# Optimization experiments

Hardware: AMD Instinct MI355X
Metric: run time of the kernel (lower is better)

## Reference

```python
import jax, jax.numpy as jnp
import numpy as np

DEPTH = 10
LAMDA = 1e-3
EPS = 1e-7


def setup_inputs() -> dict:
    key = jax.random.key(0)
    k1, k2, k3, k4 = jax.random.split(key, 4)
    B, D, O = 16384, 512, 256
    N = 2 ** DEPTH - 1        # inner nodes
    L = 2 ** DEPTH            # leaves
    data = jax.random.normal(k1, (B, D), jnp.float32)
    # small scale on W keeps sigmoid away from saturation (like nn.Linear init)
    W = jax.random.normal(k2, (N, D + 1), jnp.float32) * 0.02
    beta = jax.random.normal(k3, (N,), jnp.float32)
    param = jax.random.normal(k4, (L, O), jnp.float32)
    return {"data": data, "W": W, "beta": beta, "param": param}


def reference(data, W, beta, param):
    B = data.shape[0]
    L = param.shape[0]
    # _data_augment_: prepend constant 1 as bias feature -> [B, D+1]
    x = jnp.concatenate([jnp.ones((B, 1), data.dtype), data], axis=1)
    # inner_nodes: sigmoid(beta * linear(x)) -> [B, N]
    p = jax.nn.sigmoid(beta * (x @ W.T))
    # per-node (go-left, go-right) probabilities -> [B, N, 2]
    path_prob = jnp.stack([p, 1.0 - p], axis=2)

    mu = jnp.ones((B, 1), data.dtype)          # path prob of root
    penalty = jnp.asarray(0.0, data.dtype)
    begin = 0
    for layer in range(DEPTH):                  # fixed small loop over depth
        n = 2 ** layer
        pp = path_prob[:, begin:begin + n, :].reshape(B, 2 * n)  # [B, 2n]
        mu_rep = jnp.repeat(mu, 2, axis=1)                        # [B, 2n]
        # vectorized form of the per-node penalty loop
        alpha = jnp.sum(pp * mu_rep, axis=0) / (jnp.sum(mu_rep, axis=0) + EPS)
        alpha = jnp.clip(alpha, EPS, 1.0 - EPS)
        coeff = LAMDA * (2.0 ** (-layer))
        penalty = penalty - coeff * 0.5 * jnp.sum(jnp.log(alpha) + jnp.log(1.0 - alpha))
        mu = mu_rep * pp
        begin += n

    # mu: [B, leaf_num]; leaf_nodes: mu @ softmax(param)
    dist = jax.nn.softmax(param, axis=1)       # [L, O]
    output = mu @ dist                          # [B, O]
    # greatest_path_probability: hard argmax leaf (one-hot @ dist == gather)
    ids = jnp.argmax(mu, axis=1)
    prediction = dist[ids]                      # [B, O]
    # LogProb=True
    return (jnp.log(prediction), jnp.log(output), penalty, W)
```

## Files before the change

### kernel.cpp

```cpp
#include <hip/hip_runtime.h>
#include <hip/hip_bf16.h>

#define B_ROWS 16384
#define DDIM   512
#define NNODES 1023
#define NLEAF  1024
#define ODIM   256
#define LAMDA  1e-3
#define EPSV   1e-7f

typedef __bf16 bf16x8v __attribute__((ext_vector_type(8)));
typedef _Float16 f16x8 __attribute__((ext_vector_type(8)));
typedef float  f32x16v __attribute__((ext_vector_type(16)));

__device__ __forceinline__ float bf2f(unsigned short u) {
    return __uint_as_float(((unsigned)u) << 16);
}

__device__ __forceinline__ void gload16h(const _Float16* g, _Float16* l) {
    __builtin_amdgcn_global_load_lds(
        (const __attribute__((address_space(1))) unsigned int*)g,
        (__attribute__((address_space(3))) unsigned int*)l, 16, 0, 0);
}
__device__ __forceinline__ void gload16b(const __hip_bfloat16* g, __hip_bfloat16* l) {
    __builtin_amdgcn_global_load_lds(
        (const __attribute__((address_space(1))) unsigned int*)g,
        (__attribute__((address_space(3))) unsigned int*)l, 16, 0, 0);
}

__global__ __launch_bounds__(256)
void prep_data(const float* __restrict__ data,
               _Float16* __restrict__ Dh, _Float16* __restrict__ Dl)
{
    int idx = blockIdx.x * 256 + threadIdx.x;
    int b  = idx >> 6;
    int k8 = idx & 63;
    const float4 v0 = *reinterpret_cast<const float4*>(&data[(size_t)b * DDIM + k8 * 8]);
    const float4 v1 = *reinterpret_cast<const float4*>(&data[(size_t)b * DDIM + k8 * 8 + 4]);
    float a[8] = {v0.x, v0.y, v0.z, v0.w, v1.x, v1.y, v1.z, v1.w};
    __align__(16) _Float16 h[8], l[8];
#pragma unroll
    for (int j = 0; j < 8; ++j) {
        h[j] = (_Float16)a[j];
        l[j] = (_Float16)((a[j] - (float)h[j]) * 2048.f);
    }
    int by = b >> 7, tl = (b >> 5) & 3, ln = (b & 31) | ((k8 & 1) << 5), ks = k8 >> 1;
    size_t off = ((((size_t)by * 32 + ks) * 4 + tl) * 64 + ln) * 8;
    *reinterpret_cast<ulonglong2*>(&Dh[off]) = *reinterpret_cast<const ulonglong2*>(h);
    *reinterpret_cast<ulonglong2*>(&Dl[off]) = *reinterpret_cast<const ulonglong2*>(l);
}

__global__ __launch_bounds__(256)
void prep_w(const float* __restrict__ W,
            _Float16* __restrict__ Wh, _Float16* __restrict__ Wl)
{
    int idx = blockIdx.x * 256 + threadIdx.x;
    int t  = idx & 255;
    int ks = (idx >> 8) & 31;
    int nb = idx >> 13;
    int tm = t >> 6, ln = t & 63;
    int node = nb * 128 + tm * 32 + (ln & 31);
    int k = ks * 16 + (ln >> 5) * 8;
    __align__(16) _Float16 h[8], l[8];
    if (node < NNODES) {
#pragma unroll
        for (int j = 0; j < 8; ++j) {
            float a = W[(size_t)node * 513 + 1 + k + j];
            h[j] = (_Float16)a;
            l[j] = (_Float16)((a - (float)h[j]) * 2048.f);
        }
    } else {
#pragma unroll
        for (int j = 0; j < 8; ++j) { h[j] = (_Float16)0.f; l[j] = (_Float16)0.f; }
    }
    size_t off = (size_t)idx * 8;
    *reinterpret_cast<ulonglong2*>(&Wh[off]) = *reinterpret_cast<const ulonglong2*>(h);
    *reinterpret_cast<ulonglong2*>(&Wl[off]) = *reinterpret_cast<const ulonglong2*>(l);
}

__global__ __launch_bounds__(256, 2)
void gemm1_mfma(const _Float16* __restrict__ Wh, const _Float16* __restrict__ Wl,
                const _Float16* __restrict__ Dh, const _Float16* __restrict__ Dl,
                const float* __restrict__ W, const float* __restrict__ beta,
                float* __restrict__ PT)
{
    __shared__ _Float16 lds[2][4][4096];
    const int tid = threadIdx.x;
    const int lane = tid & 63;
    const int wv = tid >> 6;
    const int wm = wv & 1, wn = wv >> 1;
    const int id = blockIdx.x;
    const int xcd = id & 7, slot = id >> 3;
    const int bx = slot & 7;
    const int by = xcd * 16 + (slot >> 3);
    const size_t wofs = (size_t)bx * 65536 + tid * 8;
    const size_t dofs = (size_t)by * 65536 + tid * 8;
    const int t16 = tid * 8;

    f32x16v acc_h[2][2] = {};
    f32x16v acc_l[2][2] = {};

#define STAGE1(buf, tt) do { \
        const size_t so = (size_t)(tt) * 4096; \
        gload16h(Wh + wofs + so,        &lds[buf][0][t16]); \
        gload16h(Wh + wofs + so + 2048, &lds[buf][0][2048 + t16]); \
        gload16h(Wl + wofs + so,        &lds[buf][1][t16]); \
        gload16h(Wl + wofs + so + 2048, &lds[buf][1][2048 + t16]); \
        gload16h(Dh + dofs + so,        &lds[buf][2][t16]); \
        gload16h(Dh + dofs + so + 2048, &lds[buf][2][2048 + t16]); \
        gload16h(Dl + dofs + so,        &lds[buf][3][t16]); \
        gload16h(Dl + dofs + so + 2048, &lds[buf][3][2048 + t16]); \
    } while (0)

    STAGE1(0, 0);

    for (int t = 0; t < 16; ++t) {
        const int cur = t & 1;
        if (t + 1 < 16) {
            STAGE1(cur ^ 1, t + 1);
            asm volatile("s_waitcnt vmcnt(8)" ::: "memory");
        } else {
            asm volatile("s_waitcnt vmcnt(0)" ::: "memory");
        }
        __builtin_amdgcn_s_barrier();

        f16x8 ah[2][2], al[2][2], bh[2][2], bl[2][2];
#pragma unroll
        for (int kcl = 0; kcl < 2; ++kcl)
#pragma unroll
            for (int i = 0; i < 2; ++i) {
                int ao = kcl * 2048 + (wm * 2 + i) * 512 + lane * 8;
                int bo = kcl * 2048 + (wn * 2 + i) * 512 + lane * 8;
                ah[kcl][i] = *reinterpret_cast<const f16x8*>(&lds[cur][0][ao]);
                al[kcl][i] = *reinterpret_cast<const f16x8*>(&lds[cur][1][ao]);
                bh[kcl][i] = *reinterpret_cast<const f16x8*>(&lds[cur][2][bo]);
                bl[kcl][i] = *reinterpret_cast<const f16x8*>(&lds[cur][3][bo]);
            }
        __builtin_amdgcn_s_setprio(1);
#pragma unroll
        for (int kcl = 0; kcl < 2; ++kcl)
#pragma unroll
            for (int i = 0; i < 2; ++i)
#pragma unroll
                for (int j = 0; j < 2; ++j) {
                    acc_h[i][j] = __builtin_amdgcn_mfma_f32_32x32x16_f16(ah[kcl][i], bh[kcl][j], acc_h[i][j], 0, 0, 0);
                    acc_l[i][j] = __builtin_amdgcn_mfma_f32_32x32x16_f16(ah[kcl][i], bl[kcl][j], acc_l[i][j], 0, 0, 0);
                    acc_l[i][j] = __builtin_amdgcn_mfma_f32_32x32x16_f16(al[kcl][i], bh[kcl][j], acc_l[i][j], 0, 0, 0);
                }
        __builtin_amdgcn_s_setprio(0);
        asm volatile("s_waitcnt lgkmcnt(0)" ::: "memory");
        __builtin_amdgcn_s_barrier();
    }
#undef STAGE1

#pragma unroll
    for (int i = 0; i < 2; ++i) {
#pragma unroll
        for (int r = 0; r < 16; ++r) {
            int node = bx * 128 + wm * 64 + i * 32 + ((r & 3) + 8 * (r >> 2) + 4 * (lane >> 5));
            if (node < NNODES) {
                float w0 = W[(size_t)node * 513];
                float bt = beta[node];
#pragma unroll
                for (int j = 0; j < 2; ++j) {
                    float z = acc_h[i][j][r] + acc_l[i][j][r] * 4.8828125e-4f;
                    float s = bt * (z + w0);
                    float p = 1.f / (1.f + expf(-s));
                    PT[(size_t)node * B_ROWS + by * 128 + wn * 64 + j * 32 + (lane & 31)] = p;
                }
            }
        }
    }
}

__global__ __launch_bounds__(256, 4)
void tree_pass(const float* __restrict__ PT,
               __hip_bfloat16* __restrict__ MU2,
               float* __restrict__ pval,
               int*   __restrict__ pidx)
{
    const int tid = threadIdx.x;
    const int rb = blockIdx.x & 63;
    const int g  = blockIdx.x >> 6;
    const int b  = rb * 256 + tid;

    const int c4 = 15 + g;
    const int n3 = (c4 - 1) >> 1;
    const int n2 = (n3 - 1) >> 1;
    const int n1 = (n2 - 1) >> 1;
    const float pc4 = PT[(size_t)c4 * B_ROWS + b];
    const float pn3 = PT[(size_t)n3 * B_ROWS + b];
    const float pn2 = PT[(size_t)n2 * B_ROWS + b];
    const float pn1 = PT[(size_t)n1 * B_ROWS + b];
    const float pn0 = PT[b];
    float pre = ((c4 & 1) ? pn3 : 1.f - pn3)
              * ((n3 & 1) ? pn2 : 1.f - pn2)
              * ((n2 & 1) ? pn1 : 1.f - pn1)
              * ((n1 & 1) ? pn0 : 1.f - pn0);
    float root[2] = { pre * pc4, pre * (1.f - pc4) };

    __align__(16) __hip_bfloat16 mbv[64];
    float bestv = -1.f; int besti = 0;
#pragma unroll
    for (int ss = 0; ss < 2; ++ss) {
        const int t = 2 * g + ss;
        float s[32];
#pragma unroll
        for (int u = 1; u < 32; ++u) {
            int lvl = 31 - __clz(u);
            int node = ((32 << lvl) - 1) + t * (1 << lvl) + (u - (1 << lvl));
            s[u] = PT[(size_t)node * B_ROWS + b];
        }
        float w[64];
        w[1] = root[ss];
#pragma unroll
        for (int u = 1; u < 32; ++u) {
            w[2 * u]     = w[u] * s[u];
            w[2 * u + 1] = w[u] * (1.f - s[u]);
        }
#pragma unroll
        for (int q = 0; q < 32; ++q) {
            float lv = w[32 + q];
            mbv[ss * 32 + q] = __float2bfloat16(lv);
            if (lv > bestv) { bestv = lv; besti = t * 32 + q; }
        }
    }
    {
        const int mb_ = b >> 7, mt_ = (b >> 5) & 3, lnlo = b & 31;
        const ulonglong2* src = reinterpret_cast<const ulonglong2*>(mbv);
#pragma unroll
        for (int c = 0; c < 4; ++c) {
            size_t base16 = (((size_t)mb_ * 64 + g * 4 + c) * 4 + mt_) * 64;
            *reinterpret_cast<ulonglong2*>(&MU2[(base16 + lnlo) * 8])      = src[c * 2];
            *reinterpret_cast<ulonglong2*>(&MU2[(base16 + 32 + lnlo) * 8]) = src[c * 2 + 1];
        }
    }
    pval[(size_t)g * B_ROWS + b] = bestv;
    pidx[(size_t)g * B_ROWS + b] = besti;
}

__global__ __launch_bounds__(256)
void colsum(const __hip_bfloat16* __restrict__ MU2, float* __restrict__ partial)
{
    __shared__ float red[4][2][8];
    const int blk = blockIdx.x;
    const int kc = blk >> 2, mbg = blk & 3;
    const int t = threadIdx.x;
    const int w = t >> 6, ln = t & 63;
    float a[8] = {0.f, 0.f, 0.f, 0.f, 0.f, 0.f, 0.f, 0.f};
    for (int it = 0; it < 32; ++it) {
        int it2 = it * 4 + w;
        int mb = mbg * 32 + (it2 >> 2), mt = it2 & 3;
        size_t a16 = (((size_t)mb * 64 + kc) * 4 + mt) * 64 + ln;
        ulonglong2 u = *reinterpret_cast<const ulonglong2*>(&MU2[a16 * 8]);
        const unsigned short* hs = reinterpret_cast<const unsigned short*>(&u);
#pragma unroll
        for (int j = 0; j < 8; ++j) a[j] += bf2f(hs[j]);
    }
#pragma unroll
    for (int m = 1; m < 32; m <<= 1)
#pragma unroll
        for (int j = 0; j < 8; ++j) a[j] += __shfl_xor(a[j], m, 64);
    if ((ln & 31) == 0) {
#pragma unroll
        for (int j = 0; j < 8; ++j) red[w][ln >> 5][j] = a[j];
    }
    __syncthreads();
    if (t < 16) {
        float s = red[0][t >> 3][t & 7] + red[1][t >> 3][t & 7]
                + red[2][t >> 3][t & 7] + red[3][t >> 3][t & 7];
        partial[(size_t)mbg * NLEAF + kc * 16 + t] = s;
    }
}

__global__ __launch_bounds__(256)
void softmax_param(const float* __restrict__ param,
                   float* __restrict__ logdist,
                   __hip_bfloat16* __restrict__ DT2)
{
    __shared__ float red[4], red2[4];
    int l = blockIdx.x;
    int o = threadIdx.x;
    float x = param[(size_t)l * ODIM + o];
    float m = x;
#pragma unroll
    for (int s = 1; s < 64; s <<= 1) m = fmaxf(m, __shfl_xor(m, s, 64));
    if ((o & 63) == 0) red[o >> 6] = m;
    __syncthreads();
    m = fmaxf(fmaxf(red[0], red[1]), fmaxf(red[2], red[3]));
    float e = expf(x - m);
    float s = e;
#pragma unroll
    for (int k = 1; k < 64; k <<= 1) s += __shfl_xor(s, k, 64);
    if ((o & 63) == 0) red2[o >> 6] = s;
    __syncthreads();
    s = red2[0] + red2[1] + red2[2] + red2[3];
    float d = e / s;
    logdist[(size_t)l * ODIM + o] = logf(d);
    int kc = l >> 4, kk = l & 15;
    int lane = (o & 31) | ((kk >> 3) << 5);
    DT2[(((size_t)kc * 8 + (o >> 5)) * 64 + lane) * 8 + (kk & 7)] = __float2bfloat16(d);
}

__global__ __launch_bounds__(256)
void penalty_kernel(const float* __restrict__ partial, float* __restrict__ out_pen)
{
    __shared__ float M[2048];
    __shared__ double dred[256];
    int tid = threadIdx.x;
    for (int i = tid; i < 1024; i += 256)
        M[1024 + i] = partial[i] + partial[NLEAF + i] + partial[2 * NLEAF + i] + partial[3 * NLEAF + i];
    __syncthreads();
    for (int n = 512; n >= 1; n >>= 1) {
        for (int u = n + tid; u < 2 * n; u += 256) M[u] = M[2 * u] + M[2 * u + 1];
        __syncthreads();
    }
    double acc = 0.0;
    for (int u = 2 + tid; u < 2048; u += 256) {
        int lvl = 31 - __clz(u);
        float a = M[u] / (M[u >> 1] + EPSV);
        a = fminf(fmaxf(a, EPSV), 1.f - EPSV);
        float term = logf(a) + logf(1.f - a);
        acc -= ldexp((double)LAMDA * 0.5, 1 - lvl) * (double)term;
    }
    dred[tid] = acc;
    __syncthreads();
    for (int s = 128; s > 0; s >>= 1) {
        if (tid < s) dred[tid] += dred[tid + s];
        __syncthreads();
    }
    if (tid == 0) out_pen[0] = (float)dred[0];
}

__global__ __launch_bounds__(256)
void gemm2_log(const __hip_bfloat16* __restrict__ MU2,
               const __hip_bfloat16* __restrict__ DT2,
               float* __restrict__ out1)
{
    __shared__ __hip_bfloat16 ldsA[2][2048];
    __shared__ __hip_bfloat16 ldsB[2][8192];
    const int tid = threadIdx.x;
    const int lane = tid & 63;
    const int w = tid >> 6;
    const int blk = blockIdx.x;
    const int m0 = blk * 64;
    const int mb = blk >> 1;
    const int mtbase = (blk & 1) * 2;
    const int s_kcl = tid >> 7, s_mti = (tid >> 6) & 1, s_ln = tid & 63;

    f32x16v acc[2][2] = {};

#define STAGE2(buf, kc0) do { \
        size_t sa16 = (((size_t)mb * 64 + (kc0) + s_kcl) * 4 + mtbase + s_mti) * 64 + s_ln; \
        gload16b(MU2 + sa16 * 8, &ldsA[buf][tid * 8]); \
        gload16b(DT2 + ((size_t)(kc0) * 512 + tid) * 8,             &ldsB[buf][tid * 8]); \
        gload16b(DT2 + ((size_t)(kc0) * 512 + 256 + tid) * 8,       &ldsB[buf][2048 + tid * 8]); \
        gload16b(DT2 + ((size_t)((kc0) + 1) * 512 + tid) * 8,       &ldsB[buf][4096 + tid * 8]); \
        gload16b(DT2 + ((size_t)((kc0) + 1) * 512 + 256 + tid) * 8, &ldsB[buf][6144 + tid * 8]); \
    } while (0)

    STAGE2(0, 0);
    for (int it = 0; it < 32; ++it) {
        const int cur = it & 1;
        if (it + 1 < 32) {
            STAGE2(cur ^ 1, 2 * (it + 1));
            asm volatile("s_waitcnt vmcnt(5)" ::: "memory");
        } else {
            asm volatile("s_waitcnt vmcnt(0)" ::: "memory");
        }
        __builtin_amdgcn_s_barrier();
        bf16x8v a[2][2], bb[2][2];
#pragma unroll
        for (int kcl = 0; kcl < 2; ++kcl)
#pragma unroll
            for (int i = 0; i < 2; ++i) {
                a[kcl][i]  = *reinterpret_cast<const bf16x8v*>(&ldsA[cur][((kcl * 2 + i) * 64 + lane) * 8]);
                bb[kcl][i] = *reinterpret_cast<const bf16x8v*>(&ldsB[cur][((kcl * 8 + 2 * w + i) * 64 + lane) * 8]);
            }
        __builtin_amdgcn_s_setprio(1);
#pragma unroll
        for (int kcl = 0; kcl < 2; ++kcl)
#pragma unroll
            for (int i = 0; i < 2; ++i)
#pragma unroll
                for (int j = 0; j < 2; ++j)
                    acc[i][j] = __builtin_amdgcn_mfma_f32_32x32x16_bf16(a[kcl][i], bb[kcl][j], acc[i][j], 0, 0, 0);
        __builtin_amdgcn_s_setprio(0);
        asm volatile("s_waitcnt lgkmcnt(0)" ::: "memory");
        __builtin_amdgcn_s_barrier();
    }
#undef STAGE2
#pragma unroll
    for (int i = 0; i < 2; ++i)
#pragma unroll
        for (int j = 0; j < 2; ++j)
#pragma unroll
            for (int r = 0; r < 16; ++r) {
                int row = m0 + i * 32 + (r & 3) + 8 * (r >> 2) + 4 * (lane >> 5);
                int col = w * 64 + j * 32 + (lane & 31);
                out1[(size_t)row * ODIM + col] = logf(acc[i][j][r]);
            }
}

__global__ __launch_bounds__(256)
void argmax_gather(const float* __restrict__ pval, const int* __restrict__ pidx,
                   const float* __restrict__ logdist, float* __restrict__ out0)
{
    __shared__ int sid[64];
    const int blk = blockIdx.x;
    const int t = threadIdx.x;
    if (t < 64) {
        int row = blk * 64 + t;
        float bv = -1.f; int bi = 0;
        for (int g = 0; g < 16; ++g) {
            float v = pval[(size_t)g * B_ROWS + row];
            if (v > bv) { bv = v; bi = pidx[(size_t)g * B_ROWS + row]; }
        }
        sid[t] = bi;
    }
    __syncthreads();
    for (int rr = 0; rr < 64; ++rr) {
        int id = sid[rr];
        out0[(size_t)(blk * 64 + rr) * ODIM + t] = logdist[(size_t)id * ODIM + t];
    }
}

__global__ void copy_w(const float* __restrict__ W, float* __restrict__ outW)
{
    int i = blockIdx.x * 256 + threadIdx.x;
    if (i < NNODES * 513) outW[i] = W[i];
}

extern "C" void kernel_launch(void* const* d_in, const int* in_sizes, int n_in,
                              void* d_out, int out_size, void* d_ws, size_t ws_size,
                              hipStream_t stream)
{
    (void)in_sizes; (void)n_in; (void)out_size; (void)ws_size;
    const float* data  = (const float*)d_in[0];
    const float* W     = (const float*)d_in[1];
    const float* beta  = (const float*)d_in[2];
    const float* param = (const float*)d_in[3];
    float* out = (float*)d_out;

    char* ws = (char*)d_ws;
    size_t off = 0;
    float* PT = (float*)(ws + off);                   off += (size_t)NNODES * B_ROWS * 4;
    char* X = ws + off;                               off += 2 * 1048576 + 2 * 16777216;
    _Float16* Wh = (_Float16*)(X);
    _Float16* Wl = (_Float16*)(X + 1048576);
    _Float16* Dh = (_Float16*)(X + 2 * 1048576);
    _Float16* Dl = (_Float16*)(X + 2 * 1048576 + 16777216);
    __hip_bfloat16* MU2 = (__hip_bfloat16*)(X + 2 * 1048576);
    __hip_bfloat16* DT2 = (__hip_bfloat16*)(ws + off); off += (size_t)ODIM * NLEAF * 2;
    float* logdist = (float*)(ws + off);              off += (size_t)NLEAF * ODIM * 4;
    float* partial = (float*)(ws + off);              off += (size_t)4 * NLEAF * 4;
    float* pval    = (float*)(ws + off);              off += (size_t)16 * B_ROWS * 4;
    int*   pidx    = (int*)(ws + off);                off += (size_t)16 * B_ROWS * 4;

    float* out_logpred = out;
    float* out_logout  = out + (size_t)B_ROWS * ODIM;
    float* out_pen     = out + 2 * (size_t)B_ROWS * ODIM;
    float* out_W       = out_pen + 1;

    prep_data<<<4096, 256, 0, stream>>>(data, Dh, Dl);
    prep_w<<<256, 256, 0, stream>>>(W, Wh, Wl);
    softmax_param<<<NLEAF, 256, 0, stream>>>(param, logdist, DT2);

    gemm1_mfma<<<1024, 256, 0, stream>>>(Wh, Wl, Dh, Dl, W, beta, PT);

    tree_pass<<<1024, 256, 0, stream>>>(PT, MU2, pval, pidx);
    colsum<<<256, 256, 0, stream>>>(MU2, partial);
    penalty_kernel<<<1, 256, 0, stream>>>(partial, out_pen);

    gemm2_log<<<B_ROWS / 64, 256, 0, stream>>>(MU2, DT2, out_logout);
    argmax_gather<<<B_ROWS / 64, 256, 0, stream>>>(pval, pidx, logdist, out_logpred);
    copy_w<<<(NNODES * 513 + 255) / 256, 256, 0, stream>>>(W, out_W);
}
```

Baseline: 162.8 us.

## Load GEMM operands directly from global into registers, dropping LDS staging

Replaces the LDS double-buffered staging in the first GEMM with per-wave direct global loads into two register sets that alternate across k-steps. This removes shared-memory writes and reads and the block-wide barriers per iteration. In exchange, operands shared between waves are loaded redundantly from global memory through cache, and more register pressure is held for the prefetched fragments.

```diff
diff --git a/kernel.cpp b/kernel.cpp
--- a/kernel.cpp
+++ b/kernel.cpp
@@ -17,11 +17,6 @@
     return __uint_as_float(((unsigned)u) << 16);
 }
 
-__device__ __forceinline__ void gload16h(const _Float16* g, _Float16* l) {
-    __builtin_amdgcn_global_load_lds(
-        (const __attribute__((address_space(1))) unsigned int*)g,
-        (__attribute__((address_space(3))) unsigned int*)l, 16, 0, 0);
-}
 __device__ __forceinline__ void gload16b(const __hip_bfloat16* g, __hip_bfloat16* l) {
     __builtin_amdgcn_global_load_lds(
         (const __attribute__((address_space(1))) unsigned int*)g,
@@ -84,7 +79,6 @@
                 const float* __restrict__ W, const float* __restrict__ beta,
                 float* __restrict__ PT)
 {
-    __shared__ _Float16 lds[2][4][4096];
     const int tid = threadIdx.x;
     const int lane = tid & 63;
     const int wv = tid >> 6;
@@ -93,65 +87,64 @@
     const int xcd = id & 7, slot = id >> 3;
     const int bx = slot & 7;
     const int by = xcd * 16 + (slot >> 3);
-    const size_t wofs = (size_t)bx * 65536 + tid * 8;
-    const size_t dofs = (size_t)by * 65536 + tid * 8;
-    const int t16 = tid * 8;
+
+    const _Float16* qWh0 = Wh + (size_t)bx * 65536 + (wm * 2 + 0) * 512 + lane * 8;
+    const _Float16* qWh1 = Wh + (size_t)bx * 65536 + (wm * 2 + 1) * 512 + lane * 8;
+    const _Float16* qWl0 = Wl + (size_t)bx * 65536 + (wm * 2 + 0) * 512 + lane * 8;
+    const _Float16* qWl1 = Wl + (size_t)bx * 65536 + (wm * 2 + 1) * 512 + lane * 8;
+    const _Float16* qDh0 = Dh + (size_t)by * 65536 + (wn * 2 + 0) * 512 + lane * 8;
+    const _Float16* qDh1 = Dh + (size_t)by * 65536 + (wn * 2 + 1) * 512 + lane * 8;
+    const _Float16* qDl0 = Dl + (size_t)by * 65536 + (wn * 2 + 0) * 512 + lane * 8;
+    const _Float16* qDl1 = Dl + (size_t)by * 65536 + (wn * 2 + 1) * 512 + lane * 8;
 
     f32x16v acc_h[2][2] = {};
     f32x16v acc_l[2][2] = {};
 
-#define STAGE1(buf, tt) do { \
-        const size_t so = (size_t)(tt) * 4096; \
-        gload16h(Wh + wofs + so,        &lds[buf][0][t16]); \
-        gload16h(Wh + wofs + so + 2048, &lds[buf][0][2048 + t16]); \
-        gload16h(Wl + wofs + so,        &lds[buf][1][t16]); \
-        gload16h(Wl + wofs + so + 2048, &lds[buf][1][2048 + t16]); \
-        gload16h(Dh + dofs + so,        &lds[buf][2][t16]); \
-        gload16h(Dh + dofs + so + 2048, &lds[buf][2][2048 + t16]); \
-        gload16h(Dl + dofs + so,        &lds[buf][3][t16]); \
-        gload16h(Dl + dofs + so + 2048, &lds[buf][3][2048 + t16]); \
-    } while (0)
-
-    STAGE1(0, 0);
-
+    f16x8 Xah0, Xah1, Xal0, Xal1, Xbh0, Xbh1, Xbl0, Xbl1;
+    f16x8 Yah0, Yah1, Yal0, Yal1, Ybh0, Ybh1, Ybl0, Ybl1;
+
+#define LOAD8(ah0,ah1,al0,al1,bh0,bh1,bl0,bl1) do { \
+    ah0 = *reinterpret_cast<const f16x8*>(qWh0); \
+    ah1 = *reinterpret_cast<const f16x8*>(qWh1); \
+    al0 = *reinterpret_cast<const f16x8*>(qWl0); \
+    al1 = *reinterpret_cast<const f16x8*>(qWl1); \
+    bh0 = *reinterpret_cast<const f16x8*>(qDh0); \
+    bh1 = *reinterpret_cast<const f16x8*>(qDh1); \
+    bl0 = *reinterpret_cast<const f16x8*>(qDl0); \
+    bl1 = *reinterpret_cast<const f16x8*>(qDl1); \
+    qWh0 += 2048; qWh1 += 2048; qWl0 += 2048; qWl1 += 2048; \
+    qDh0 += 2048; qDh1 += 2048; qDl0 += 2048; qDl1 += 2048; \
+} while (0)
+
+#define MFMA12(ah0,ah1,al0,al1,bh0,bh1,bl0,bl1) do { \
+    acc_h[0][0] = __builtin_amdgcn_mfma_f32_32x32x16_f16(ah0, bh0, acc_h[0][0], 0, 0, 0); \
+    acc_h[0][1] = __builtin_amdgcn_mfma_f32_32x32x16_f16(ah0, bh1, acc_h[0][1], 0, 0, 0); \
+    acc_h[1][0] = __builtin_amdgcn_mfma_f32_32x32x16_f16(ah1, bh0, acc_h[1][0], 0, 0, 0); \
+    acc_h[1][1] = __builtin_amdgcn_mfma_f32_32x32x16_f16(ah1, bh1, acc_h[1][1], 0, 0, 0); \
+    acc_l[0][0] = __builtin_amdgcn_mfma_f32_32x32x16_f16(ah0, bl0, acc_l[0][0], 0, 0, 0); \
+    acc_l[0][1] = __builtin_amdgcn_mfma_f32_32x32x16_f16(ah0, bl1, acc_l[0][1], 0, 0, 0); \
+    acc_l[1][0] = __builtin_amdgcn_mfma_f32_32x32x16_f16(ah1, bl0, acc_l[1][0], 0, 0, 0); \
+    acc_l[1][1] = __builtin_amdgcn_mfma_f32_32x32x16_f16(ah1, bl1, acc_l[1][1], 0, 0, 0); \
+    acc_l[0][0] = __builtin_amdgcn_mfma_f32_32x32x16_f16(al0, bh0, acc_l[0][0], 0, 0, 0); \
+    acc_l[0][1] = __builtin_amdgcn_mfma_f32_32x32x16_f16(al0, bh1, acc_l[0][1], 0, 0, 0); \
+    acc_l[1][0] = __builtin_amdgcn_mfma_f32_32x32x16_f16(al1, bh0, acc_l[1][0], 0, 0, 0); \
+    acc_l[1][1] = __builtin_amdgcn_mfma_f32_32x32x16_f16(al1, bh1, acc_l[1][1], 0, 0, 0); \
+} while (0)
+
+    LOAD8(Xah0, Xah1, Xal0, Xal1, Xbh0, Xbh1, Xbl0, Xbl1);
     for (int t = 0; t < 16; ++t) {
-        const int cur = t & 1;
-        if (t + 1 < 16) {
-            STAGE1(cur ^ 1, t + 1);
-            asm volatile("s_waitcnt vmcnt(8)" ::: "memory");
-        } else {
-            asm volatile("s_waitcnt vmcnt(0)" ::: "memory");
-        }
-        __builtin_amdgcn_s_barrier();
-
-        f16x8 ah[2][2], al[2][2], bh[2][2], bl[2][2];
-#pragma unroll
-        for (int kcl = 0; kcl < 2; ++kcl)
-#pragma unroll
-            for (int i = 0; i < 2; ++i) {
-                int ao = kcl * 2048 + (wm * 2 + i) * 512 + lane * 8;
-                int bo = kcl * 2048 + (wn * 2 + i) * 512 + lane * 8;
-                ah[kcl][i] = *reinterpret_cast<const f16x8*>(&lds[cur][0][ao]);
-                al[kcl][i] = *reinterpret_cast<const f16x8*>(&lds[cur][1][ao]);
-                bh[kcl][i] = *reinterpret_cast<const f16x8*>(&lds[cur][2][bo]);
-                bl[kcl][i] = *reinterpret_cast<const f16x8*>(&lds[cur][3][bo]);
-            }
+        LOAD8(Yah0, Yah1, Yal0, Yal1, Ybh0, Ybh1, Ybl0, Ybl1);
         __builtin_amdgcn_s_setprio(1);
-#pragma unroll
-        for (int kcl = 0; kcl < 2; ++kcl)
-#pragma unroll
-            for (int i = 0; i < 2; ++i)
-#pragma unroll
-                for (int j = 0; j < 2; ++j) {
-                    acc_h[i][j] = __builtin_amdgcn_mfma_f32_32x32x16_f16(ah[kcl][i], bh[kcl][j], acc_h[i][j], 0, 0, 0);
-                    acc_l[i][j] = __builtin_amdgcn_mfma_f32_32x32x16_f16(ah[kcl][i], bl[kcl][j], acc_l[i][j], 0, 0, 0);
-                    acc_l[i][j] = __builtin_amdgcn_mfma_f32_32x32x16_f16(al[kcl][i], bh[kcl][j], acc_l[i][j], 0, 0, 0);
-                }
+        MFMA12(Xah0, Xah1, Xal0, Xal1, Xbh0, Xbh1, Xbl0, Xbl1);
         __builtin_amdgcn_s_setprio(0);
-        asm volatile("s_waitcnt lgkmcnt(0)" ::: "memory");
-        __builtin_amdgcn_s_barrier();
-    }
-#undef STAGE1
+        if (t < 15)
+            LOAD8(Xah0, Xah1, Xal0, Xal1, Xbh0, Xbh1, Xbl0, Xbl1);
+        __builtin_amdgcn_s_setprio(1);
+        MFMA12(Yah0, Yah1, Yal0, Yal1, Ybh0, Ybh1, Ybl0, Ybl1);
+        __builtin_amdgcn_s_setprio(0);
+    }
+#undef LOAD8
+#undef MFMA12
 
 #pragma unroll
     for (int i = 0; i < 2; ++i) {
```

Result: slower. 169.5 us (+4.1%).

## Merge prep kernels and load data low-part directly into registers in GEMM1

Applied to the files above, without the earlier changes.

Fuses the two conversion kernels into a single launch that dispatches on block index. In the split-fp16 GEMM, the low part of the data operand is no longer staged through LDS. Each wave loads its own fragment straight from global memory into registers, prefetched one iteration ahead, which shrinks LDS use and LDS read traffic. In exchange it adds direct global loads (possibly redundant across waves sharing the same columns), extra registers, and a more delicate vmcnt accounting.

```diff
diff --git a/kernel.cpp b/kernel.cpp
--- a/kernel.cpp
+++ b/kernel.cpp
@@ -29,53 +29,51 @@
 }
 
 __global__ __launch_bounds__(256)
-void prep_data(const float* __restrict__ data,
-               _Float16* __restrict__ Dh, _Float16* __restrict__ Dl)
-{
-    int idx = blockIdx.x * 256 + threadIdx.x;
-    int b  = idx >> 6;
-    int k8 = idx & 63;
-    const float4 v0 = *reinterpret_cast<const float4*>(&data[(size_t)b * DDIM + k8 * 8]);
-    const float4 v1 = *reinterpret_cast<const float4*>(&data[(size_t)b * DDIM + k8 * 8 + 4]);
-    float a[8] = {v0.x, v0.y, v0.z, v0.w, v1.x, v1.y, v1.z, v1.w};
-    __align__(16) _Float16 h[8], l[8];
-#pragma unroll
-    for (int j = 0; j < 8; ++j) {
-        h[j] = (_Float16)a[j];
-        l[j] = (_Float16)((a[j] - (float)h[j]) * 2048.f);
-    }
-    int by = b >> 7, tl = (b >> 5) & 3, ln = (b & 31) | ((k8 & 1) << 5), ks = k8 >> 1;
-    size_t off = ((((size_t)by * 32 + ks) * 4 + tl) * 64 + ln) * 8;
-    *reinterpret_cast<ulonglong2*>(&Dh[off]) = *reinterpret_cast<const ulonglong2*>(h);
-    *reinterpret_cast<ulonglong2*>(&Dl[off]) = *reinterpret_cast<const ulonglong2*>(l);
-}
-
-__global__ __launch_bounds__(256)
-void prep_w(const float* __restrict__ W,
-            _Float16* __restrict__ Wh, _Float16* __restrict__ Wl)
-{
-    int idx = blockIdx.x * 256 + threadIdx.x;
-    int t  = idx & 255;
-    int ks = (idx >> 8) & 31;
-    int nb = idx >> 13;
-    int tm = t >> 6, ln = t & 63;
-    int node = nb * 128 + tm * 32 + (ln & 31);
-    int k = ks * 16 + (ln >> 5) * 8;
-    __align__(16) _Float16 h[8], l[8];
-    if (node < NNODES) {
+void prep_all(const float* __restrict__ data, const float* __restrict__ W,
+              _Float16* __restrict__ Dh, _Float16* __restrict__ Dl,
+              _Float16* __restrict__ Wh, _Float16* __restrict__ Wl)
+{
+    if (blockIdx.x < 4096) {
+        int idx = blockIdx.x * 256 + threadIdx.x;
+        int b  = idx >> 6;
+        int k8 = idx & 63;
+        const float4 v0 = *reinterpret_cast<const float4*>(&data[(size_t)b * DDIM + k8 * 8]);
+        const float4 v1 = *reinterpret_cast<const float4*>(&data[(size_t)b * DDIM + k8 * 8 + 4]);
+        float a[8] = {v0.x, v0.y, v0.z, v0.w, v1.x, v1.y, v1.z, v1.w};
+        __align__(16) _Float16 h[8], l[8];
 #pragma unroll
         for (int j = 0; j < 8; ++j) {
-            float a = W[(size_t)node * 513 + 1 + k + j];
-            h[j] = (_Float16)a;
-            l[j] = (_Float16)((a - (float)h[j]) * 2048.f);
-        }
+            h[j] = (_Float16)a[j];
+            l[j] = (_Float16)((a[j] - (float)h[j]) * 2048.f);
+        }
+        int by = b >> 7, tl = (b >> 5) & 3, ln = (b & 31) | ((k8 & 1) << 5), ks = k8 >> 1;
+        size_t off = ((((size_t)by * 32 + ks) * 4 + tl) * 64 + ln) * 8;
+        *reinterpret_cast<ulonglong2*>(&Dh[off]) = *reinterpret_cast<const ulonglong2*>(h);
+        *reinterpret_cast<ulonglong2*>(&Dl[off]) = *reinterpret_cast<const ulonglong2*>(l);
     } else {
-#pragma unroll
-        for (int j = 0; j < 8; ++j) { h[j] = (_Float16)0.f; l[j] = (_Float16)0.f; }
-    }
-    size_t off = (size_t)idx * 8;
-    *reinterpret_cast<ulonglong2*>(&Wh[off]) = *reinterpret_cast<const ulonglong2*>(h);
-    *reinterpret_cast<ulonglong2*>(&Wl[off]) = *reinterpret_cast<const ulonglong2*>(l);
+        int idx = (blockIdx.x - 4096) * 256 + threadIdx.x;
+        int t  = idx & 255;
+        int ks = (idx >> 8) & 31;
+        int nb = idx >> 13;
+        int tm = t >> 6, ln = t & 63;
+        int node = nb * 128 + tm * 32 + (ln & 31);
+        int k = ks * 16 + (ln >> 5) * 8;
+        __align__(16) _Float16 h[8], l[8];
+        if (node < NNODES) {
+#pragma unroll
+            for (int j = 0; j < 8; ++j) {
+                float a = W[(size_t)node * 513 + 1 + k + j];
+                h[j] = (_Float16)a;
+                l[j] = (_Float16)((a - (float)h[j]) * 2048.f);
+            }
+        } else {
+#pragma unroll
+            for (int j = 0; j < 8; ++j) { h[j] = (_Float16)0.f; l[j] = (_Float16)0.f; }
+        }
+        size_t off = (size_t)idx * 8;
+        *reinterpret_cast<ulonglong2*>(&Wh[off]) = *reinterpret_cast<const ulonglong2*>(h);
+        *reinterpret_cast<ulonglong2*>(&Wl[off]) = *reinterpret_cast<const ulonglong2*>(l);
+    }
 }
 
 __global__ __launch_bounds__(256, 2)
@@ -84,7 +82,7 @@
                 const float* __restrict__ W, const float* __restrict__ beta,
                 float* __restrict__ PT)
 {
-    __shared__ _Float16 lds[2][4][4096];
+    __shared__ _Float16 lds[2][3][4096];
     const int tid = threadIdx.x;
     const int lane = tid & 63;
     const int wv = tid >> 6;
@@ -96,11 +94,12 @@
     const size_t wofs = (size_t)bx * 65536 + tid * 8;
     const size_t dofs = (size_t)by * 65536 + tid * 8;
     const int t16 = tid * 8;
+    const _Float16* dlp = Dl + (size_t)by * 65536 + (wn * 2) * 512 + lane * 8;
 
     f32x16v acc_h[2][2] = {};
     f32x16v acc_l[2][2] = {};
 
-#define STAGE1(buf, tt) do { \
+#define STAGE6(buf, tt) do { \
         const size_t so = (size_t)(tt) * 4096; \
         gload16h(Wh + wofs + so,        &lds[buf][0][t16]); \
         gload16h(Wh + wofs + so + 2048, &lds[buf][0][2048 + t16]); \
@@ -108,23 +107,34 @@
         gload16h(Wl + wofs + so + 2048, &lds[buf][1][2048 + t16]); \
         gload16h(Dh + dofs + so,        &lds[buf][2][t16]); \
         gload16h(Dh + dofs + so + 2048, &lds[buf][2][2048 + t16]); \
-        gload16h(Dl + dofs + so,        &lds[buf][3][t16]); \
-        gload16h(Dl + dofs + so + 2048, &lds[buf][3][2048 + t16]); \
     } while (0)
 
-    STAGE1(0, 0);
+    f16x8 Xdl[2][2], Ydl[2][2];
+
+    STAGE6(0, 0);
+#pragma unroll
+    for (int kcl = 0; kcl < 2; ++kcl)
+#pragma unroll
+        for (int j = 0; j < 2; ++j)
+            Xdl[kcl][j] = *reinterpret_cast<const f16x8*>(dlp + kcl * 2048 + j * 512);
 
     for (int t = 0; t < 16; ++t) {
         const int cur = t & 1;
         if (t + 1 < 16) {
-            STAGE1(cur ^ 1, t + 1);
-            asm volatile("s_waitcnt vmcnt(8)" ::: "memory");
+            STAGE6(cur ^ 1, t + 1);
+#pragma unroll
+            for (int kcl = 0; kcl < 2; ++kcl)
+#pragma unroll
+                for (int j = 0; j < 2; ++j)
+                    Ydl[kcl][j] = *reinterpret_cast<const f16x8*>(
+                        dlp + (size_t)(t + 1) * 4096 + kcl * 2048 + j * 512);
+            asm volatile("s_waitcnt vmcnt(10)" ::: "memory");
         } else {
             asm volatile("s_waitcnt vmcnt(0)" ::: "memory");
         }
         __builtin_amdgcn_s_barrier();
 
-        f16x8 ah[2][2], al[2][2], bh[2][2], bl[2][2];
+        f16x8 ah[2][2], al[2][2], bh[2][2];
 #pragma unroll
         for (int kcl = 0; kcl < 2; ++kcl)
 #pragma unroll
@@ -134,7 +144,6 @@
                 ah[kcl][i] = *reinterpret_cast<const f16x8*>(&lds[cur][0][ao]);
                 al[kcl][i] = *reinterpret_cast<const f16x8*>(&lds[cur][1][ao]);
                 bh[kcl][i] = *reinterpret_cast<const f16x8*>(&lds[cur][2][bo]);
-                bl[kcl][i] = *reinterpret_cast<const f16x8*>(&lds[cur][3][bo]);
             }
         __builtin_amdgcn_s_setprio(1);
 #pragma unroll
@@ -144,14 +153,19 @@
 #pragma unroll
                 for (int j = 0; j < 2; ++j) {
                     acc_h[i][j] = __builtin_amdgcn_mfma_f32_32x32x16_f16(ah[kcl][i], bh[kcl][j], acc_h[i][j], 0, 0, 0);
-                    acc_l[i][j] = __builtin_amdgcn_mfma_f32_32x32x16_f16(ah[kcl][i], bl[kcl][j], acc_l[i][j], 0, 0, 0);
+                    acc_l[i][j] = __builtin_amdgcn_mfma_f32_32x32x16_f16(ah[kcl][i], Xdl[kcl][j], acc_l[i][j], 0, 0, 0);
                     acc_l[i][j] = __builtin_amdgcn_mfma_f32_32x32x16_f16(al[kcl][i], bh[kcl][j], acc_l[i][j], 0, 0, 0);
                 }
         __builtin_amdgcn_s_setprio(0);
         asm volatile("s_waitcnt lgkmcnt(0)" ::: "memory");
         __builtin_amdgcn_s_barrier();
-    }
-#undef STAGE1
+#pragma unroll
+        for (int kcl = 0; kcl < 2; ++kcl)
+#pragma unroll
+            for (int j = 0; j < 2; ++j)
+                Xdl[kcl][j] = Ydl[kcl][j];
+    }
+#undef STAGE6
 
 #pragma unroll
     for (int i = 0; i < 2; ++i) {
@@ -462,8 +476,7 @@
     float* out_pen     = out + 2 * (size_t)B_ROWS * ODIM;
     float* out_W       = out_pen + 1;
 
-    prep_data<<<4096, 256, 0, stream>>>(data, Dh, Dl);
-    prep_w<<<256, 256, 0, stream>>>(W, Wh, Wl);
+    prep_all<<<4352, 256, 0, stream>>>(data, W, Dh, Dl, Wh, Wl);
     softmax_param<<<NLEAF, 256, 0, stream>>>(param, logdist, DT2);
 
     gemm1_mfma<<<1024, 256, 0, stream>>>(Wh, Wl, Dh, Dl, W, beta, PT);
```

Result: slower. 174.1 us (+7.0%).

## Enlarge GEMM1 tile to 128x256 with 512 threads and fuse prep kernels

Applied to the files above, without the earlier changes.

The gate GEMM now uses 512-thread blocks, each covering 256 batch rows instead of 128, so every W tile staged in LDS is reused across twice as many rows and the grid halves to 512 blocks. The data prep layout is changed to match the wider tile, and the LDS pipeline is restructured so compute on the current buffer overlaps the next tile's loads with a single wait per step. The prep_data, prep_w and copy_w kernels are merged into one launch to cut launch overhead. In exchange each block needs more LDS and registers, which may lower occupancy, and the smaller grid may leave some CUs less evenly loaded.

```diff
diff --git a/kernel.cpp b/kernel.cpp
--- a/kernel.cpp
+++ b/kernel.cpp
@@ -29,62 +29,64 @@
 }
 
 __global__ __launch_bounds__(256)
-void prep_data(const float* __restrict__ data,
-               _Float16* __restrict__ Dh, _Float16* __restrict__ Dl)
-{
-    int idx = blockIdx.x * 256 + threadIdx.x;
-    int b  = idx >> 6;
-    int k8 = idx & 63;
-    const float4 v0 = *reinterpret_cast<const float4*>(&data[(size_t)b * DDIM + k8 * 8]);
-    const float4 v1 = *reinterpret_cast<const float4*>(&data[(size_t)b * DDIM + k8 * 8 + 4]);
-    float a[8] = {v0.x, v0.y, v0.z, v0.w, v1.x, v1.y, v1.z, v1.w};
-    __align__(16) _Float16 h[8], l[8];
-#pragma unroll
-    for (int j = 0; j < 8; ++j) {
-        h[j] = (_Float16)a[j];
-        l[j] = (_Float16)((a[j] - (float)h[j]) * 2048.f);
-    }
-    int by = b >> 7, tl = (b >> 5) & 3, ln = (b & 31) | ((k8 & 1) << 5), ks = k8 >> 1;
-    size_t off = ((((size_t)by * 32 + ks) * 4 + tl) * 64 + ln) * 8;
-    *reinterpret_cast<ulonglong2*>(&Dh[off]) = *reinterpret_cast<const ulonglong2*>(h);
-    *reinterpret_cast<ulonglong2*>(&Dl[off]) = *reinterpret_cast<const ulonglong2*>(l);
-}
-
-__global__ __launch_bounds__(256)
-void prep_w(const float* __restrict__ W,
-            _Float16* __restrict__ Wh, _Float16* __restrict__ Wl)
-{
-    int idx = blockIdx.x * 256 + threadIdx.x;
-    int t  = idx & 255;
-    int ks = (idx >> 8) & 31;
-    int nb = idx >> 13;
-    int tm = t >> 6, ln = t & 63;
-    int node = nb * 128 + tm * 32 + (ln & 31);
-    int k = ks * 16 + (ln >> 5) * 8;
-    __align__(16) _Float16 h[8], l[8];
-    if (node < NNODES) {
+void prep_all(const float* __restrict__ data, const float* __restrict__ W,
+              _Float16* __restrict__ Dh, _Float16* __restrict__ Dl,
+              _Float16* __restrict__ Wh, _Float16* __restrict__ Wl,
+              float* __restrict__ outW)
+{
+    if (blockIdx.x < 4096) {
+        int idx = blockIdx.x * 256 + threadIdx.x;
+        int b  = idx >> 6;
+        int k8 = idx & 63;
+        const float4 v0 = *reinterpret_cast<const float4*>(&data[(size_t)b * DDIM + k8 * 8]);
+        const float4 v1 = *reinterpret_cast<const float4*>(&data[(size_t)b * DDIM + k8 * 8 + 4]);
+        float a[8] = {v0.x, v0.y, v0.z, v0.w, v1.x, v1.y, v1.z, v1.w};
+        __align__(16) _Float16 h[8], l[8];
 #pragma unroll
         for (int j = 0; j < 8; ++j) {
-            float a = W[(size_t)node * 513 + 1 + k + j];
-            h[j] = (_Float16)a;
-            l[j] = (_Float16)((a - (float)h[j]) * 2048.f);
-        }
+            h[j] = (_Float16)a[j];
+            l[j] = (_Float16)((a[j] - (float)h[j]) * 2048.f);
+        }
+        int by = b >> 8, tl = (b >> 5) & 7, ln = (b & 31) | ((k8 & 1) << 5), ks = k8 >> 1;
+        size_t off = ((((size_t)by * 32 + ks) * 8 + tl) * 64 + ln) * 8;
+        *reinterpret_cast<ulonglong2*>(&Dh[off]) = *reinterpret_cast<const ulonglong2*>(h);
+        *reinterpret_cast<ulonglong2*>(&Dl[off]) = *reinterpret_cast<const ulonglong2*>(l);
+    } else if (blockIdx.x < 4352) {
+        int idx = (blockIdx.x - 4096) * 256 + threadIdx.x;
+        int t  = idx & 255;
+        int ks = (idx >> 8) & 31;
+        int nb = idx >> 13;
+        int tm = t >> 6, ln = t & 63;
+        int node = nb * 128 + tm * 32 + (ln & 31);
+        int k = ks * 16 + (ln >> 5) * 8;
+        __align__(16) _Float16 h[8], l[8];
+        if (node < NNODES) {
+#pragma unroll
+            for (int j = 0; j < 8; ++j) {
+                float a = W[(size_t)node * 513 + 1 + k + j];
+                h[j] = (_Float16)a;
+                l[j] = (_Float16)((a - (float)h[j]) * 2048.f);
+            }
+        } else {
+#pragma unroll
+            for (int j = 0; j < 8; ++j) { h[j] = (_Float16)0.f; l[j] = (_Float16)0.f; }
+        }
+        size_t off = (size_t)idx * 8;
+        *reinterpret_cast<ulonglong2*>(&Wh[off]) = *reinterpret_cast<const ulonglong2*>(h);
+        *reinterpret_cast<ulonglong2*>(&Wl[off]) = *reinterpret_cast<const ulonglong2*>(l);
     } else {
-#pragma unroll
-        for (int j = 0; j < 8; ++j) { h[j] = (_Float16)0.f; l[j] = (_Float16)0.f; }
-    }
-    size_t off = (size_t)idx * 8;
-    *reinterpret_cast<ulonglong2*>(&Wh[off]) = *reinterpret_cast<const ulonglong2*>(h);
-    *reinterpret_cast<ulonglong2*>(&Wl[off]) = *reinterpret_cast<const ulonglong2*>(l);
-}
-
-__global__ __launch_bounds__(256, 2)
+        int i = (blockIdx.x - 4352) * 256 + threadIdx.x;
+        if (i < NNODES * 513) outW[i] = W[i];
+    }
+}
+
+__global__ __launch_bounds__(512, 2)
 void gemm1_mfma(const _Float16* __restrict__ Wh, const _Float16* __restrict__ Wl,
                 const _Float16* __restrict__ Dh, const _Float16* __restrict__ Dl,
                 const float* __restrict__ W, const float* __restrict__ beta,
                 float* __restrict__ PT)
 {
-    __shared__ _Float16 lds[2][4][4096];
+    __shared__ _Float16 lds[2][24576];
     const int tid = threadIdx.x;
     const int lane = tid & 63;
     const int wv = tid >> 6;
@@ -92,66 +94,62 @@
     const int id = blockIdx.x;
     const int xcd = id & 7, slot = id >> 3;
     const int bx = slot & 7;
-    const int by = xcd * 16 + (slot >> 3);
+    const int by = xcd * 8 + (slot >> 3);
     const size_t wofs = (size_t)bx * 65536 + tid * 8;
-    const size_t dofs = (size_t)by * 65536 + tid * 8;
-    const int t16 = tid * 8;
+    const size_t dofs = (size_t)by * 131072 + tid * 8;
 
     f32x16v acc_h[2][2] = {};
     f32x16v acc_l[2][2] = {};
 
-#define STAGE1(buf, tt) do { \
-        const size_t so = (size_t)(tt) * 4096; \
-        gload16h(Wh + wofs + so,        &lds[buf][0][t16]); \
-        gload16h(Wh + wofs + so + 2048, &lds[buf][0][2048 + t16]); \
-        gload16h(Wl + wofs + so,        &lds[buf][1][t16]); \
-        gload16h(Wl + wofs + so + 2048, &lds[buf][1][2048 + t16]); \
-        gload16h(Dh + dofs + so,        &lds[buf][2][t16]); \
-        gload16h(Dh + dofs + so + 2048, &lds[buf][2][2048 + t16]); \
-        gload16h(Dl + dofs + so,        &lds[buf][3][t16]); \
-        gload16h(Dl + dofs + so + 2048, &lds[buf][3][2048 + t16]); \
+#define STAGE(buf, tt) do { \
+        const size_t wo = wofs + (size_t)(tt) * 4096; \
+        const size_t dd = dofs + (size_t)(tt) * 8192; \
+        gload16h(Wh + wo,        &lds[buf][tid * 8]); \
+        gload16h(Wl + wo,        &lds[buf][4096  + tid * 8]); \
+        gload16h(Dh + dd,        &lds[buf][8192  + tid * 8]); \
+        gload16h(Dh + dd + 4096, &lds[buf][12288 + tid * 8]); \
+        gload16h(Dl + dd,        &lds[buf][16384 + tid * 8]); \
+        gload16h(Dl + dd + 4096, &lds[buf][20480 + tid * 8]); \
     } while (0)
 
-    STAGE1(0, 0);
+    STAGE(0, 0);
+    asm volatile("s_waitcnt vmcnt(0)" ::: "memory");
+    __builtin_amdgcn_s_barrier();
 
     for (int t = 0; t < 16; ++t) {
         const int cur = t & 1;
-        if (t + 1 < 16) {
-            STAGE1(cur ^ 1, t + 1);
-            asm volatile("s_waitcnt vmcnt(8)" ::: "memory");
-        } else {
-            asm volatile("s_waitcnt vmcnt(0)" ::: "memory");
-        }
+        if (t < 15) STAGE(cur ^ 1, t + 1);
+        const _Float16* L = lds[cur];
+#pragma unroll
+        for (int kcl = 0; kcl < 2; ++kcl) {
+            f16x8 ah[2], al[2], bh[2], bl[2];
+#pragma unroll
+            for (int i = 0; i < 2; ++i) {
+                int ao = ((kcl * 4 + wm * 2 + i) * 64 + lane) * 8;
+                ah[i] = *reinterpret_cast<const f16x8*>(&L[ao]);
+                al[i] = *reinterpret_cast<const f16x8*>(&L[4096 + ao]);
+            }
+#pragma unroll
+            for (int j = 0; j < 2; ++j) {
+                int bo = ((kcl * 8 + wn * 2 + j) * 64 + lane) * 8;
+                bh[j] = *reinterpret_cast<const f16x8*>(&L[8192 + bo]);
+                bl[j] = *reinterpret_cast<const f16x8*>(&L[16384 + bo]);
+            }
+            __builtin_amdgcn_s_setprio(1);
+#pragma unroll
+            for (int i = 0; i < 2; ++i)
+#pragma unroll
+                for (int j = 0; j < 2; ++j) {
+                    acc_h[i][j] = __builtin_amdgcn_mfma_f32_32x32x16_f16(ah[i], bh[j], acc_h[i][j], 0, 0, 0);
+                    acc_l[i][j] = __builtin_amdgcn_mfma_f32_32x32x16_f16(ah[i], bl[j], acc_l[i][j], 0, 0, 0);
+                    acc_l[i][j] = __builtin_amdgcn_mfma_f32_32x32x16_f16(al[i], bh[j], acc_l[i][j], 0, 0, 0);
+                }
+            __builtin_amdgcn_s_setprio(0);
+        }
+        if (t < 15) asm volatile("s_waitcnt vmcnt(0)" ::: "memory");
         __builtin_amdgcn_s_barrier();
-
-        f16x8 ah[2][2], al[2][2], bh[2][2], bl[2][2];
-#pragma unroll
-        for (int kcl = 0; kcl < 2; ++kcl)
-#pragma unroll
-            for (int i = 0; i < 2; ++i) {
-                int ao = kcl * 2048 + (wm * 2 + i) * 512 + lane * 8;
-                int bo = kcl * 2048 + (wn * 2 + i) * 512 + lane * 8;
-                ah[kcl][i] = *reinterpret_cast<const f16x8*>(&lds[cur][0][ao]);
-                al[kcl][i] = *reinterpret_cast<const f16x8*>(&lds[cur][1][ao]);
-                bh[kcl][i] = *reinterpret_cast<const f16x8*>(&lds[cur][2][bo]);
-                bl[kcl][i] = *reinterpret_cast<const f16x8*>(&lds[cur][3][bo]);
-            }
-        __builtin_amdgcn_s_setprio(1);
-#pragma unroll
-        for (int kcl = 0; kcl < 2; ++kcl)
-#pragma unroll
-            for (int i = 0; i < 2; ++i)
-#pragma unroll
-                for (int j = 0; j < 2; ++j) {
-                    acc_h[i][j] = __builtin_amdgcn_mfma_f32_32x32x16_f16(ah[kcl][i], bh[kcl][j], acc_h[i][j], 0, 0, 0);
-                    acc_l[i][j] = __builtin_amdgcn_mfma_f32_32x32x16_f16(ah[kcl][i], bl[kcl][j], acc_l[i][j], 0, 0, 0);
-                    acc_l[i][j] = __builtin_amdgcn_mfma_f32_32x32x16_f16(al[kcl][i], bh[kcl][j], acc_l[i][j], 0, 0, 0);
-                }
-        __builtin_amdgcn_s_setprio(0);
-        asm volatile("s_waitcnt lgkmcnt(0)" ::: "memory");
-        __builtin_amdgcn_s_barrier();
-    }
-#undef STAGE1
+    }
+#undef STAGE
 
 #pragma unroll
     for (int i = 0; i < 2; ++i) {
@@ -166,7 +164,7 @@
                     float z = acc_h[i][j][r] + acc_l[i][j][r] * 4.8828125e-4f;
                     float s = bt * (z + w0);
                     float p = 1.f / (1.f + expf(-s));
-                    PT[(size_t)node * B_ROWS + by * 128 + wn * 64 + j * 32 + (lane & 31)] = p;
+                    PT[(size_t)node * B_ROWS + by * 256 + wn * 64 + j * 32 + (lane & 31)] = p;
                 }
             }
         }
@@ -425,12 +423,6 @@
     }
 }
 
-__global__ void copy_w(const float* __restrict__ W, float* __restrict__ outW)
-{
-    int i = blockIdx.x * 256 + threadIdx.x;
-    if (i < NNODES * 513) outW[i] = W[i];
-}
-
 extern "C" void kernel_launch(void* const* d_in, const int* in_sizes, int n_in,
                               void* d_out, int out_size, void* d_ws, size_t ws_size,
                               hipStream_t stream)
@@ -462,11 +454,10 @@
     float* out_pen     = out + 2 * (size_t)B_ROWS * ODIM;
     float* out_W       = out_pen + 1;
 
-    prep_data<<<4096, 256, 0, stream>>>(data, Dh, Dl);
-    prep_w<<<256, 256, 0, stream>>>(W, Wh, Wl);
+    prep_all<<<6404, 256, 0, stream>>>(data, W, Dh, Dl, Wh, Wl, out_W);
     softmax_param<<<NLEAF, 256, 0, stream>>>(param, logdist, DT2);
 
-    gemm1_mfma<<<1024, 256, 0, stream>>>(Wh, Wl, Dh, Dl, W, beta, PT);
+    gemm1_mfma<<<512, 512, 0, stream>>>(Wh, Wl, Dh, Dl, W, beta, PT);
 
     tree_pass<<<1024, 256, 0, stream>>>(PT, MU2, pval, pidx);
     colsum<<<256, 256, 0, stream>>>(MU2, partial);
@@ -474,5 +465,4 @@
 
     gemm2_log<<<B_ROWS / 64, 256, 0, stream>>>(MU2, DT2, out_logout);
     argmax_gather<<<B_ROWS / 64, 256, 0, stream>>>(pval, pidx, logdist, out_logpred);
-    copy_w<<<(NNODES * 513 + 255) / 256, 256, 0, stream>>>(W, out_W);
-}
+}
```

Measured after the change: 162.0 us. About the same (-0.5%).
